# Kernel optimization log

Hardware: AMD Instinct MI355X
Metric: run time of the kernel (lower is better)

The kernel has to match this reference:

```python
import jax, jax.numpy as jnp
import numpy as np

_EPS = 1e-4  # pytorch3d se3_exp_map clamps the SQUARED rotation angle at this eps


def _hat(w):
    # w: [..., 3] -> skew-symmetric [..., 3, 3]
    wx, wy, wz = w[..., 0], w[..., 1], w[..., 2]
    z = jnp.zeros_like(wx)
    return jnp.stack([
        jnp.stack([z, -wz, wy], axis=-1),
        jnp.stack([wz, z, -wx], axis=-1),
        jnp.stack([-wy, wx, z], axis=-1),
    ], axis=-2)


def _se3_exp(dofs):
    # dofs: [..., 6] = (log_translation, log_rotation), pytorch3d convention.
    # Returns R [..., 3, 3] and t [..., 3] such that p' = R @ p + t,
    # matching pytorch3d's row-convention matrix M ([:3,:3]=R^T, [3,:3]=t)
    # applied as p' = p @ M[:3,:3] + M[3,:3].
    t_log = dofs[..., :3]
    w = dofs[..., 3:]
    nrms = jnp.sum(w * w, axis=-1)
    theta = jnp.sqrt(jnp.clip(nrms, _EPS))  # [...]
    H = _hat(w)
    H2 = H @ H
    st, ct = jnp.sin(theta), jnp.cos(theta)
    f1 = (st / theta)[..., None, None]
    f2 = ((1.0 - ct) / (theta * theta))[..., None, None]
    f3 = ((theta - st) / (theta * theta * theta))[..., None, None]
    I = jnp.eye(3, dtype=dofs.dtype)
    R = I + f1 * H + f2 * H2            # Rodrigues
    V = I + f2 * H + f3 * H2            # left-Jacobian of SO(3)
    t = jnp.einsum('...ij,...j->...i', V, t_log)
    return R, t


def setup_inputs() -> dict:
    key = jax.random.key(0)
    k1, k2 = jax.random.split(key)
    B, T, N = 64, 28, 4096
    X_v = jax.random.normal(k1, (B, T, N, 3), dtype=jnp.float32)
    dofs = jax.random.normal(k2, (B, T, 6), dtype=jnp.float32)
    return {"X_v": X_v, "dofs": dofs}


def reference(X_v, dofs):
    # Fused, fully-batched version of the per-tooth python loop:
    # one SE3 exp over all (B,T) transforms + one batched point transform.
    R, t = _se3_exp(dofs)                                  # [B,T,3,3], [B,T,3]
    out = jnp.einsum('btij,btnj->btni', R, X_v) + t[:, :, None, :]
    return out
```

## Files before the change

kernel.cpp:

```cpp
#include <hip/hip_runtime.h>


__global__ __launch_bounds__(256) void se3_apply_kernel(
    const float* __restrict__ X,
    const float* __restrict__ dofs,
    float* __restrict__ out,
    int n3,
    int tilesPerBT)
{
    __shared__ float lds[3072];

    const int bt   = blockIdx.x / tilesPerBT;
    const int tile = blockIdx.x - bt * tilesPerBT;
    const int t    = threadIdx.x;

    const long long baseF = (long long)bt * (long long)n3 + (long long)tile * 3072;
    const int f4InBT   = tile * 768;
    const int n4       = n3 >> 2;
    const float4* __restrict__ Xp = (const float4*)(X + baseF);
    float4* __restrict__ Op       = (float4*)(out + baseF);
    float4* lds4 = (float4*)lds;

    float4 v0, v1, v2;
    const bool g0 = (f4InBT + t        ) < n4;
    const bool g1 = (f4InBT + t + 256  ) < n4;
    const bool g2 = (f4InBT + t + 512  ) < n4;
    if (g0) v0 = Xp[t];
    if (g1) v1 = Xp[t + 256];
    if (g2) v2 = Xp[t + 512];

    const float* d = dofs + bt * 6;
    const float tx = d[0], ty = d[1], tz = d[2];
    const float wx = d[3], wy = d[4], wz = d[5];

    const float nrm2  = wx * wx + wy * wy + wz * wz;
    const float th2   = fmaxf(nrm2, 1e-4f);
    const float theta = sqrtf(th2);
    const float st = sinf(theta);
    const float ct = cosf(theta);
    const float f1 = st / theta;
    const float f2 = (1.0f - ct) / th2;
    const float f3 = (theta - st) / (th2 * theta);

    const float xx = wx * wx, yy = wy * wy, zz = wz * wz;
    const float xy = wx * wy, xz = wx * wz, yz = wy * wz;

    const float R00 = 1.0f - f2 * (yy + zz);
    const float R01 = f2 * xy - f1 * wz;
    const float R02 = f2 * xz + f1 * wy;
    const float R10 = f2 * xy + f1 * wz;
    const float R11 = 1.0f - f2 * (xx + zz);
    const float R12 = f2 * yz - f1 * wx;
    const float R20 = f2 * xz - f1 * wy;
    const float R21 = f2 * yz + f1 * wx;
    const float R22 = 1.0f - f2 * (xx + yy);

    const float V00 = 1.0f - f3 * (yy + zz);
    const float V01 = f3 * xy - f2 * wz;
    const float V02 = f3 * xz + f2 * wy;
    const float V10 = f3 * xy + f2 * wz;
    const float V11 = 1.0f - f3 * (xx + zz);
    const float V12 = f3 * yz - f2 * wx;
    const float V20 = f3 * xz - f2 * wy;
    const float V21 = f3 * yz + f2 * wx;
    const float V22 = 1.0f - f3 * (xx + yy);

    const float Tx = V00 * tx + V01 * ty + V02 * tz;
    const float Ty = V10 * tx + V11 * ty + V12 * tz;
    const float Tz = V20 * tx + V21 * ty + V22 * tz;

    if (g0) lds4[t]       = v0;
    if (g1) lds4[t + 256] = v1;
    if (g2) lds4[t + 512] = v2;
    __syncthreads();

#pragma unroll
    for (int j = 0; j < 4; ++j) {
        const int p = 3 * (t + 256 * j);
        const float px = lds[p + 0];
        const float py = lds[p + 1];
        const float pz = lds[p + 2];
        lds[p + 0] = fmaf(R00, px, fmaf(R01, py, fmaf(R02, pz, Tx)));
        lds[p + 1] = fmaf(R10, px, fmaf(R11, py, fmaf(R12, pz, Ty)));
        lds[p + 2] = fmaf(R20, px, fmaf(R21, py, fmaf(R22, pz, Tz)));
    }
    __syncthreads();

    if (g0) Op[t]       = lds4[t];
    if (g1) Op[t + 256] = lds4[t + 256];
    if (g2) Op[t + 512] = lds4[t + 512];
}

extern "C" void kernel_launch(void* const* d_in, const int* in_sizes, int n_in,
                              void* d_out, int out_size, void* d_ws, size_t ws_size,
                              hipStream_t stream) {
    const float* X    = (const float*)d_in[0];
    const float* dofs = (const float*)d_in[1];
    float* out        = (float*)d_out;

    const int BT = in_sizes[1] / 6;
    const int n3 = in_sizes[0] / BT;

    const int tilesPerBT = (n3 + 3071) / 3072;

    dim3 grid((unsigned)(BT * tilesPerBT));
    se3_apply_kernel<<<grid, 256, 0, stream>>>(X, dofs, out, n3, tilesPerBT);
}
```

Baseline: 156.2 us.

## Load four points per thread directly, dropping the LDS staging transpose

Each thread now loads three contiguous float4s holding four xyz points and transforms them in registers, so the LDS round trip and both block barriers go away. The rotation and translation values are passed through readfirstlane so they live in scalar registers. Global accesses become strided by 48 bytes per lane instead of fully coalesced, which could reduce memory efficiency, and a scalar fallback loop handles partial tiles.

```diff
diff --git a/kernel.cpp b/kernel.cpp
--- a/kernel.cpp
+++ b/kernel.cpp
@@ -1,5 +1,9 @@
 #include <hip/hip_runtime.h>
 
+
+__device__ __forceinline__ float rfl(float x) {
+    return __uint_as_float(__builtin_amdgcn_readfirstlane(__float_as_uint(x)));
+}
 
 __global__ __launch_bounds__(256) void se3_apply_kernel(
     const float* __restrict__ X,
@@ -8,26 +12,18 @@
     int n3,
     int tilesPerBT)
 {
-    __shared__ float lds[3072];
-
     const int bt   = blockIdx.x / tilesPerBT;
     const int tile = blockIdx.x - bt * tilesPerBT;
     const int t    = threadIdx.x;
 
-    const long long baseF = (long long)bt * (long long)n3 + (long long)tile * 3072;
-    const int f4InBT   = tile * 768;
-    const int n4       = n3 >> 2;
+    const int fInBT = tile * 3072 + t * 12;
+    const long long baseF = (long long)bt * (long long)n3 + (long long)fInBT;
     const float4* __restrict__ Xp = (const float4*)(X + baseF);
     float4* __restrict__ Op       = (float4*)(out + baseF);
-    float4* lds4 = (float4*)lds;
 
+    const bool full = (fInBT + 12) <= n3;
     float4 v0, v1, v2;
-    const bool g0 = (f4InBT + t        ) < n4;
-    const bool g1 = (f4InBT + t + 256  ) < n4;
-    const bool g2 = (f4InBT + t + 512  ) < n4;
-    if (g0) v0 = Xp[t];
-    if (g1) v1 = Xp[t + 256];
-    if (g2) v2 = Xp[t + 512];
+    if (full) { v0 = Xp[0]; v1 = Xp[1]; v2 = Xp[2]; }
 
     const float* d = dofs + bt * 6;
     const float tx = d[0], ty = d[1], tz = d[2];
@@ -45,15 +41,15 @@
     const float xx = wx * wx, yy = wy * wy, zz = wz * wz;
     const float xy = wx * wy, xz = wx * wz, yz = wy * wz;
 
-    const float R00 = 1.0f - f2 * (yy + zz);
-    const float R01 = f2 * xy - f1 * wz;
-    const float R02 = f2 * xz + f1 * wy;
-    const float R10 = f2 * xy + f1 * wz;
-    const float R11 = 1.0f - f2 * (xx + zz);
-    const float R12 = f2 * yz - f1 * wx;
-    const float R20 = f2 * xz - f1 * wy;
-    const float R21 = f2 * yz + f1 * wx;
-    const float R22 = 1.0f - f2 * (xx + yy);
+    const float R00 = rfl(1.0f - f2 * (yy + zz));
+    const float R01 = rfl(f2 * xy - f1 * wz);
+    const float R02 = rfl(f2 * xz + f1 * wy);
+    const float R10 = rfl(f2 * xy + f1 * wz);
+    const float R11 = rfl(1.0f - f2 * (xx + zz));
+    const float R12 = rfl(f2 * yz - f1 * wx);
+    const float R20 = rfl(f2 * xz - f1 * wy);
+    const float R21 = rfl(f2 * yz + f1 * wx);
+    const float R22 = rfl(1.0f - f2 * (xx + yy));
 
     const float V00 = 1.0f - f3 * (yy + zz);
     const float V01 = f3 * xy - f2 * wz;
@@ -65,30 +61,40 @@
     const float V21 = f3 * yz + f2 * wx;
     const float V22 = 1.0f - f3 * (xx + yy);
 
-    const float Tx = V00 * tx + V01 * ty + V02 * tz;
-    const float Ty = V10 * tx + V11 * ty + V12 * tz;
-    const float Tz = V20 * tx + V21 * ty + V22 * tz;
+    const float Tx = rfl(V00 * tx + V01 * ty + V02 * tz);
+    const float Ty = rfl(V10 * tx + V11 * ty + V12 * tz);
+    const float Tz = rfl(V20 * tx + V21 * ty + V22 * tz);
 
-    if (g0) lds4[t]       = v0;
-    if (g1) lds4[t + 256] = v1;
-    if (g2) lds4[t + 512] = v2;
-    __syncthreads();
+    if (full) {
+        const float x0 = v0.x, y0 = v0.y, z0 = v0.z;
+        const float x1 = v0.w, y1 = v1.x, z1 = v1.y;
+        const float x2 = v1.z, y2 = v1.w, z2 = v2.x;
+        const float x3 = v2.y, y3 = v2.z, z3 = v2.w;
 
-#pragma unroll
-    for (int j = 0; j < 4; ++j) {
-        const int p = 3 * (t + 256 * j);
-        const float px = lds[p + 0];
-        const float py = lds[p + 1];
-        const float pz = lds[p + 2];
-        lds[p + 0] = fmaf(R00, px, fmaf(R01, py, fmaf(R02, pz, Tx)));
-        lds[p + 1] = fmaf(R10, px, fmaf(R11, py, fmaf(R12, pz, Ty)));
-        lds[p + 2] = fmaf(R20, px, fmaf(R21, py, fmaf(R22, pz, Tz)));
+        float4 o0, o1, o2;
+        o0.x = fmaf(R00, x0, fmaf(R01, y0, fmaf(R02, z0, Tx)));
+        o0.y = fmaf(R10, x0, fmaf(R11, y0, fmaf(R12, z0, Ty)));
+        o0.z = fmaf(R20, x0, fmaf(R21, y0, fmaf(R22, z0, Tz)));
+        o0.w = fmaf(R00, x1, fmaf(R01, y1, fmaf(R02, z1, Tx)));
+        o1.x = fmaf(R10, x1, fmaf(R11, y1, fmaf(R12, z1, Ty)));
+        o1.y = fmaf(R20, x1, fmaf(R21, y1, fmaf(R22, z1, Tz)));
+        o1.z = fmaf(R00, x2, fmaf(R01, y2, fmaf(R02, z2, Tx)));
+        o1.w = fmaf(R10, x2, fmaf(R11, y2, fmaf(R12, z2, Ty)));
+        o2.x = fmaf(R20, x2, fmaf(R21, y2, fmaf(R22, z2, Tz)));
+        o2.y = fmaf(R00, x3, fmaf(R01, y3, fmaf(R02, z3, Tx)));
+        o2.z = fmaf(R10, x3, fmaf(R11, y3, fmaf(R12, z3, Ty)));
+        o2.w = fmaf(R20, x3, fmaf(R21, y3, fmaf(R22, z3, Tz)));
+
+        Op[0] = o0; Op[1] = o1; Op[2] = o2;
+    } else {
+        for (int f = fInBT; f + 3 <= n3; f += 3) {
+            const long long g = (long long)bt * (long long)n3 + f;
+            const float px = X[g + 0], py = X[g + 1], pz = X[g + 2];
+            out[g + 0] = fmaf(R00, px, fmaf(R01, py, fmaf(R02, pz, Tx)));
+            out[g + 1] = fmaf(R10, px, fmaf(R11, py, fmaf(R12, pz, Ty)));
+            out[g + 2] = fmaf(R20, px, fmaf(R21, py, fmaf(R22, pz, Tz)));
+        }
     }
-    __syncthreads();
-
-    if (g0) Op[t]       = lds4[t];
-    if (g1) Op[t + 256] = lds4[t + 256];
-    if (g2) Op[t + 512] = lds4[t + 512];
 }
 
 extern "C" void kernel_launch(void* const* d_in, const int* in_sizes, int n_in,
```

Result: no change. 158.5 us (+1.4%).
